# Performance work log

Hardware: AMD Instinct MI355X
Metric: run time of the kernel (lower is better)

The kernel has to match this reference:

```python
import jax, jax.numpy as jnp
import numpy as np

ALPHA_MEM = 0.95      # util.decayconst(tau_mem)
ALPHA_MEM_OUT = 0.95  # util.decayconst(tau_mem_out)
ALPHA_P = 0.99        # util.decayconst(tau_p)
SURR_SCALE = 100.0

@jax.custom_vjp
def spike(x):
    # Heaviside forward, surrogate gradient backward (SurrGradSpike)
    return (x > 0).astype(x.dtype)

def _spike_fwd(x):
    return spike(x), x

def _spike_bwd(x, g):
    return (g / (SURR_SCALE * jnp.abs(x) + 1.0) ** 2,)

spike.defvjp(_spike_fwd, _spike_bwd)


def setup_inputs() -> dict:
    B, T, N, NIN, NOUT, D = 64, 400, 1024, 128, 32, 3
    key = jax.random.key(0)
    ks = jax.random.split(key, 8)
    inputs = jax.random.normal(ks[0], (B, T, NIN), dtype=jnp.float32)
    w = jax.random.normal(ks[1], (N, N), dtype=jnp.float32) / np.sqrt(N).astype(np.float32)
    w_in = jax.random.normal(ks[2], (NIN, N), dtype=jnp.float32) * np.float32(0.3 / np.sqrt(NIN))
    w_out = jax.random.normal(ks[3], (N, NOUT), dtype=jnp.float32) * np.float32(0.3 / np.sqrt(N))
    w_signs = jnp.where(jax.random.uniform(ks[4], (N,)) < 0.8, 1.0, -1.0).astype(jnp.float32)
    dmap = (jax.random.uniform(ks[5], (D, N, N)) < 0.2).astype(jnp.float32)  # delay-wise connectivity mask
    p = jax.random.uniform(ks[6], (N,), minval=-0.5, maxval=0.5).astype(jnp.float32)
    delays = jnp.array([1, 2, 4], dtype=jnp.int32)
    return dict(inputs=inputs, w=w, w_in=w_in, w_out=w_out, w_signs=w_signs,
                dmap=dmap, p=p, delays=delays)


def _forward(inputs, w, w_in, w_out, w_signs, dmap, p, delays):
    B, T, _ = inputs.shape
    N = w.shape[0]
    L = int(np.max(np.asarray(delays))) + 1  # ring-buffer length (static)
    dtype = inputs.dtype

    inp = jnp.einsum('btc,cn->btn', inputs, w_in)           # epoch.input, (B,T,N)
    W = dmap * (w_signs[:, None] * jnp.abs(w))[None]        # (D,N,N)
    depr = (p < 0).astype(dtype)                            # p_depr_mask

    def step(carry, inp_t):
        mem, w_p, buf_out, buf_wp, t = carry
        out = spike(mem - 1.0)                              # mark_spikes
        buf_out = buf_out.at[t % L].set(out)                # record_state
        buf_wp = buf_wp.at[t % L].set(w_p)
        idx = (t - delays) % L
        syn_p = buf_out[idx] * (1.0 + buf_wp[idx])          # (D,B,N)
        syn = jnp.einsum('dbe,deo->bo', syn_p, W)
        w_p_new = w_p * ALPHA_P + out * p * (1.0 + depr * w_p)
        mem_new = ALPHA_MEM * mem + inp_t + syn - jax.lax.stop_gradient(out)
        return (mem_new, w_p_new, buf_out, buf_wp, t + 1), out

    z = jnp.zeros((B, N), dtype)
    bufs = jnp.zeros((L, B, N), dtype)
    carry0 = (z, z, bufs, bufs, jnp.int32(0))
    _, out_rec = jax.lax.scan(step, carry0, jnp.swapaxes(inp, 0, 1))  # (T,B,N)

    # compute_readout: leaky integrator over projected spikes
    h2 = jnp.einsum('tbn,no->tbo', out_rec, w_out)
    def ro_step(r, h):
        r = ALPHA_MEM_OUT * r + h
        return r, r
    _, readout = jax.lax.scan(ro_step, jnp.zeros((B, w_out.shape[1]), dtype), h2)
    return jnp.swapaxes(readout, 0, 1)                      # (B,T,NOUT)


def reference(inputs, w, w_in, w_out, w_signs, dmap, p, delays):
    return _forward(inputs, w, w_in, w_out, w_signs, dmap, p, delays)
```

## Files before the change

### kernel.cpp

```cpp
#include <hip/hip_runtime.h>
#include <cstdint>
#include <cstddef>

#define BB    64
#define TT    400
#define NN    1024
#define NIN   128
#define NOUT  32
#define DD    3
#define LL6   6
#define GG    16
#define BPG   4
#define NT    32
#define KK    3072
#define CAP   800

#define ALPHA_MEM     0.95f
#define ALPHA_MEM_OUT 0.95f
#define ALPHA_P       0.99f

__global__ void build_W(const float* __restrict__ w,
                        const float* __restrict__ w_signs,
                        const float* __restrict__ dmap,
                        float* __restrict__ W) {
    int idx = blockIdx.x * blockDim.x + threadIdx.x;
    if (idx >= DD * NN * NN) return;
    int en = idx % (NN * NN);
    int e  = en / NN;
    W[idx] = dmap[idx] * (w_signs[e] * fabsf(w[en]));
}

__global__ void build_csr(const float* __restrict__ W,
                          uint2* __restrict__ pack,
                          int*   __restrict__ ccnt) {
    const int col = blockIdx.x;
    const int tid = threadIdx.x;
    __shared__ int pref[256];
    __shared__ int total_s;

    int cnt = 0;
    #pragma unroll
    for (int i = 0; i < 12; ++i) {
        const float v = W[(size_t)(tid * 12 + i) * NN + col];
        cnt += (v != 0.0f) ? 1 : 0;
    }
    pref[tid] = cnt;
    __syncthreads();
    if (tid == 0) {
        int run = 0;
        for (int j = 0; j < 256; ++j) { int c = pref[j]; pref[j] = run; run += c; }
        total_s = run;
        ccnt[col] = (run > CAP) ? CAP : run;
    }
    __syncthreads();

    int ofs = pref[tid];
    #pragma unroll
    for (int i = 0; i < 12; ++i) {
        const int k = tid * 12 + i;
        const float v = W[(size_t)k * NN + col];
        if (v != 0.0f && ofs < CAP) {
            pack[(size_t)col * CAP + ofs] = make_uint2((unsigned)k, __float_as_uint(v));
            ++ofs;
        }
    }
    for (int s = total_s + tid; s < CAP; s += 256)
        pack[(size_t)col * CAP + s] = make_uint2(0u, 0u);
}

__global__ void gemm_in(const float* __restrict__ inputs,
                        const float* __restrict__ w_in,
                        float* __restrict__ inp) {
    int idx = blockIdx.x * blockDim.x + threadIdx.x;
    if (idx >= TT * BB * NN) return;
    int n  = idx & (NN - 1);
    int tb = idx >> 10;
    int b  = tb & 63;
    int t  = tb >> 6;
    const float* row = inputs + ((size_t)b * TT + t) * NIN;
    float acc = 0.0f;
    #pragma unroll 8
    for (int c = 0; c < NIN; ++c)
        acc = fmaf(row[c], w_in[c * NN + n], acc);
    inp[idx] = acc;
}

__global__ void zero_sc1(float* __restrict__ p, int n) {
    int i = blockIdx.x * blockDim.x + threadIdx.x;
    if (i < n)
        __hip_atomic_store(p + i, 0.0f, __ATOMIC_RELAXED, __HIP_MEMORY_SCOPE_AGENT);
}

__global__ __launch_bounds__(256, 2) void snn_scan(
    const float* __restrict__ inputs,
    const float* __restrict__ w_in,
    const float* __restrict__ w_out,
    const float* __restrict__ p,
    const int*   __restrict__ delays,
    const float* __restrict__ W,
    const float* __restrict__ w_raw,
    const float* __restrict__ w_signs,
    const float* __restrict__ dmap,
    float*       __restrict__ ring,
    int*         __restrict__ cnt,
    float*       __restrict__ hpart,
    const float* __restrict__ inp_pre,
    const uint2* __restrict__ pack,
    const int*   __restrict__ ccnt,
    float*       __restrict__ out,
    int use_pre, int use_W, int use_csr)
{
    __shared__ __align__(16) float sa[KK * BPG];
    __shared__ float w_out_s[32 * NOUT];
    __shared__ float spk_s[BPG * 32];
    __shared__ float s_sign[NN];
    __shared__ float s_in[BPG * NIN];

    const int bid  = blockIdx.x;
    const int g    = bid >> 5;
    const int tile = bid & 31;
    const int tid  = threadIdx.x;
    const int lane = tid & 63;
    const int wv   = tid >> 6;

    const bool st = (tid < BPG * 32);
    const int  sb = tid >> 5;
    const int  nl = tid & 31;

    const int gks = tid >> 3;
    const int gcg = tid & 7;

    const int colg = tid >> 3;
    const int sub  = tid & 7;

    float mem = 0.0f, wp = 0.0f, r = 0.0f;
    float pn = 0.0f, depr = 0.0f;
    if (st) { pn = p[tile * 32 + nl]; depr = (pn < 0.0f) ? 1.0f : 0.0f; }

    const int d0 = delays[0], d1 = delays[1], d2 = delays[2];

    for (int k = tid; k < 32 * NOUT; k += 256)
        w_out_s[k] = w_out[(tile * 32 + (k >> 5)) * NOUT + (k & 31)];
    if (!use_W)
        for (int k = tid; k < NN; k += 256) s_sign[k] = w_signs[k];
    __syncthreads();

    const float* Wt = W     + tile * 32 + gcg * 4;
    const float* Dt = dmap  + tile * 32 + gcg * 4;
    const float* Rt = w_raw + tile * 32 + gcg * 4;
    const uint2* Pk = pack  + (size_t)(tile * 32 + colg) * CAP;
    int niter = 0;
    if (use_csr) niter = (ccnt[tile * 32 + colg] + 7) >> 3;

    for (int t = 0; t < TT; ++t) {
        const int slot_w = t % LL6;
        const int s0 = (t - d0 + 2 * LL6) % LL6;
        const int s1 = (t - d1 + 2 * LL6) % LL6;
        const int s2 = (t - d2 + 2 * LL6) % LL6;

        bool  spk = false;
        float ia  = 0.0f;
        if (st) {
            spk = (mem - 1.0f) > 0.0f;
            const float a = spk ? (1.0f + wp) : 0.0f;
            __hip_atomic_store(ring + (((size_t)slot_w * BB + g * BPG + sb) << 10)
                                    + tile * 32 + nl,
                               a, __ATOMIC_RELAXED, __HIP_MEMORY_SCOPE_AGENT);
            wp = ALPHA_P * wp + (spk ? pn * (1.0f + depr * wp) : 0.0f);
            spk_s[tid] = spk ? 1.0f : 0.0f;
            if (use_pre)
                ia = inp_pre[((size_t)t * BB + g * BPG + sb) * NN + tile * 32 + nl];
        }
        if (!use_pre) {
            for (int k = tid; k < BPG * NIN; k += 256) {
                int b2 = k >> 7, c = k & 127;
                s_in[k] = inputs[((size_t)(g * BPG + b2) * TT + t) * NIN + c];
            }
        }
        __syncthreads();

        if (st) {
            float h = 0.0f;
            #pragma unroll
            for (int n2 = 0; n2 < 32; ++n2)
                h = fmaf(spk_s[sb * 32 + n2], w_out_s[n2 * 32 + nl], h);
            __hip_atomic_store(hpart + ((((size_t)(t & 1) * NT + tile) * BB)
                                        + g * BPG + sb) * NOUT + nl,
                               h, __ATOMIC_RELAXED, __HIP_MEMORY_SCOPE_AGENT);
            if (!use_pre) {
                #pragma unroll 8
                for (int c = 0; c < NIN; ++c)
                    ia = fmaf(s_in[sb * NIN + c], w_in[c * NN + tile * 32 + nl], ia);
            }
        }
        __syncthreads();

        if (tid == 0)
            __hip_atomic_fetch_add(&cnt[g * 32], 1, __ATOMIC_RELEASE,
                                   __HIP_MEMORY_SCOPE_AGENT);

        {
            const int b2 = lane >> 4;
            const int eo = lane & 15;
            #pragma unroll 16
            for (int i = 0; i < 48; ++i) {
                const int c  = i * 4 + wv;
                const int kl = c * 16 + eo;
                const int d  = kl >> 10;
                const int e  = kl & 1023;
                const int sl = (d == 0) ? s0 : ((d == 1) ? s1 : s2);
                const float v = __hip_atomic_load(
                    ring + (((size_t)sl * BB + g * BPG + b2) << 10) + e,
                    __ATOMIC_RELAXED, __HIP_MEMORY_SCOPE_AGENT);
                sa[kl * 4 + b2] = v;
            }
        }
        __syncthreads();

        if (tid == 0) {
            const int target = 32 * (t + 1);
            while (__hip_atomic_load(&cnt[g * 32], __ATOMIC_ACQUIRE,
                                     __HIP_MEMORY_SCOPE_AGENT) < target)
                __builtin_amdgcn_s_sleep(2);
        }
        __syncthreads();

        if (tile == 0 && st) {
            float h = 0.0f;
            #pragma unroll
            for (int k3 = 0; k3 < NT; ++k3)
                h += __hip_atomic_load(hpart + ((((size_t)(t & 1) * NT + k3) * BB)
                                                + g * BPG + sb) * NOUT + nl,
                                       __ATOMIC_RELAXED, __HIP_MEMORY_SCOPE_AGENT);
            r = ALPHA_MEM_OUT * r + h;
            out[((size_t)(g * BPG + sb) * TT + t) * NOUT + nl] = r;
        }

        if (use_csr) {
            float a0 = 0.0f, a1 = 0.0f, a2 = 0.0f, a3 = 0.0f;
            #pragma unroll 4
            for (int i = 0; i < niter; ++i) {
                const uint2 pv = Pk[i * 8 + sub];
                const float v  = __uint_as_float(pv.y);
                const float4 av = *(const float4*)&sa[pv.x << 2];
                a0 = fmaf(av.x, v, a0);
                a1 = fmaf(av.y, v, a1);
                a2 = fmaf(av.z, v, a2);
                a3 = fmaf(av.w, v, a3);
            }
            __syncthreads();

            float* red = sa;
            red[(colg * 4 + 0) * 9 + sub] = a0;
            red[(colg * 4 + 1) * 9 + sub] = a1;
            red[(colg * 4 + 2) * 9 + sub] = a2;
            red[(colg * 4 + 3) * 9 + sub] = a3;
            __syncthreads();

            if (st) {
                float syn = 0.0f;
                #pragma unroll
                for (int k2 = 0; k2 < 8; ++k2)
                    syn += red[(nl * 4 + sb) * 9 + k2];
                mem = ALPHA_MEM * mem + ia + syn - (spk ? 1.0f : 0.0f);
            }
            __syncthreads();
        } else {
            float4 acc0 = {0,0,0,0}, acc1 = {0,0,0,0}, acc2 = {0,0,0,0}, acc3 = {0,0,0,0};
            if (use_W) {
                #pragma unroll 8
                for (int i = 0; i < 96; ++i) {
                    const int kk = gks + (i << 5);
                    const float4 av = *(const float4*)&sa[kk << 2];
                    const float4 wv4 = *(const float4*)(Wt + ((size_t)kk << 10));
                    acc0.x = fmaf(av.x, wv4.x, acc0.x); acc0.y = fmaf(av.x, wv4.y, acc0.y);
                    acc0.z = fmaf(av.x, wv4.z, acc0.z); acc0.w = fmaf(av.x, wv4.w, acc0.w);
                    acc1.x = fmaf(av.y, wv4.x, acc1.x); acc1.y = fmaf(av.y, wv4.y, acc1.y);
                    acc1.z = fmaf(av.y, wv4.z, acc1.z); acc1.w = fmaf(av.y, wv4.w, acc1.w);
                    acc2.x = fmaf(av.z, wv4.x, acc2.x); acc2.y = fmaf(av.z, wv4.y, acc2.y);
                    acc2.z = fmaf(av.z, wv4.z, acc2.z); acc2.w = fmaf(av.z, wv4.w, acc2.w);
                    acc3.x = fmaf(av.w, wv4.x, acc3.x); acc3.y = fmaf(av.w, wv4.y, acc3.y);
                    acc3.z = fmaf(av.w, wv4.z, acc3.z); acc3.w = fmaf(av.w, wv4.w, acc3.w);
                }
            } else {
                #pragma unroll 2
                for (int i = 0; i < 96; ++i) {
                    const int kk = gks + (i << 5);
                    const int e  = kk & 1023;
                    const float sg = s_sign[e];
                    const float4 dm = *(const float4*)(Dt + ((size_t)kk << 10));
                    const float4 wr = *(const float4*)(Rt + ((size_t)e << 10));
                    float4 wv4;
                    wv4.x = dm.x * (sg * fabsf(wr.x));
                    wv4.y = dm.y * (sg * fabsf(wr.y));
                    wv4.z = dm.z * (sg * fabsf(wr.z));
                    wv4.w = dm.w * (sg * fabsf(wr.w));
                    const float4 av = *(const float4*)&sa[kk << 2];
                    acc0.x = fmaf(av.x, wv4.x, acc0.x); acc0.y = fmaf(av.x, wv4.y, acc0.y);
                    acc0.z = fmaf(av.x, wv4.z, acc0.z); acc0.w = fmaf(av.x, wv4.w, acc0.w);
                    acc1.x = fmaf(av.y, wv4.x, acc1.x); acc1.y = fmaf(av.y, wv4.y, acc1.y);
                    acc1.z = fmaf(av.y, wv4.z, acc1.z); acc1.w = fmaf(av.y, wv4.w, acc1.w);
                    acc2.x = fmaf(av.z, wv4.x, acc2.x); acc2.y = fmaf(av.z, wv4.y, acc2.y);
                    acc2.z = fmaf(av.z, wv4.z, acc2.z); acc2.w = fmaf(av.z, wv4.w, acc2.w);
                    acc3.x = fmaf(av.w, wv4.x, acc3.x); acc3.y = fmaf(av.w, wv4.y, acc3.y);
                    acc3.z = fmaf(av.w, wv4.z, acc3.z); acc3.w = fmaf(av.w, wv4.w, acc3.w);
                }
            }
            __syncthreads();

            float* red = sa;
            {
                const int o0 = gcg * 4;
                red[(0 * 32 + o0 + 0) * 33 + gks] = acc0.x;
                red[(0 * 32 + o0 + 1) * 33 + gks] = acc0.y;
                red[(0 * 32 + o0 + 2) * 33 + gks] = acc0.z;
                red[(0 * 32 + o0 + 3) * 33 + gks] = acc0.w;
                red[(1 * 32 + o0 + 0) * 33 + gks] = acc1.x;
                red[(1 * 32 + o0 + 1) * 33 + gks] = acc1.y;
                red[(1 * 32 + o0 + 2) * 33 + gks] = acc1.z;
                red[(1 * 32 + o0 + 3) * 33 + gks] = acc1.w;
                red[(2 * 32 + o0 + 0) * 33 + gks] = acc2.x;
                red[(2 * 32 + o0 + 1) * 33 + gks] = acc2.y;
                red[(2 * 32 + o0 + 2) * 33 + gks] = acc2.z;
                red[(2 * 32 + o0 + 3) * 33 + gks] = acc2.w;
                red[(3 * 32 + o0 + 0) * 33 + gks] = acc3.x;
                red[(3 * 32 + o0 + 1) * 33 + gks] = acc3.y;
                red[(3 * 32 + o0 + 2) * 33 + gks] = acc3.z;
                red[(3 * 32 + o0 + 3) * 33 + gks] = acc3.w;
            }
            __syncthreads();

            if (st) {
                float syn = 0.0f;
                #pragma unroll
                for (int k2 = 0; k2 < 32; ++k2)
                    syn += red[tid * 33 + k2];
                mem = ALPHA_MEM * mem + ia + syn - (spk ? 1.0f : 0.0f);
            }
            __syncthreads();
        }
    }
}

extern "C" void kernel_launch(void* const* d_in, const int* in_sizes, int n_in,
                              void* d_out, int out_size, void* d_ws, size_t ws_size,
                              hipStream_t stream) {
    const float* inputs  = (const float*)d_in[0];
    const float* w       = (const float*)d_in[1];
    const float* w_in    = (const float*)d_in[2];
    const float* w_out   = (const float*)d_in[3];
    const float* w_signs = (const float*)d_in[4];
    const float* dmap    = (const float*)d_in[5];
    const float* p       = (const float*)d_in[6];
    const int*   delays  = (const int*)d_in[7];
    float*       outp    = (float*)d_out;

    const size_t ring_f = (size_t)LL6 * BB * NN;
    const size_t cnt_f  = GG * 32;
    const size_t hp_f   = (size_t)2 * NT * BB * NOUT;
    const size_t W_f    = (size_t)DD * NN * NN;
    const size_t pre_f  = (size_t)TT * BB * NN;
    const size_t csr_f  = (size_t)NN * CAP * 2;
    const size_t cc_f   = NN;

    float* ws = (float*)d_ws;
    float* ring  = ws;
    int*   cntp  = (int*)(ws + ring_f);
    float* hpart = ws + ring_f + cnt_f;
    size_t used  = ring_f + cnt_f + hp_f;

    int use_W = 0, use_pre = 0, use_csr = 0;
    float *W = nullptr, *inp_pre = nullptr;
    uint2 *pack = nullptr;
    int   *ccnt = nullptr;
    if (ws_size >= (used + W_f) * 4)   { use_W = 1;   W = ws + used;       used += W_f; }
    if (ws_size >= (used + pre_f) * 4) { use_pre = 1; inp_pre = ws + used; used += pre_f; }
    if (use_W && ws_size >= (used + csr_f + cc_f) * 4) {
        use_csr = 1;
        pack = (uint2*)(ws + used); used += csr_f;
        ccnt = (int*)(ws + used);   used += cc_f;
    }

    if (use_W) {
        const int total = DD * NN * NN;
        build_W<<<(total + 255) / 256, 256, 0, stream>>>(w, w_signs, dmap, W);
    }
    if (use_csr)
        build_csr<<<NN, 256, 0, stream>>>(W, pack, ccnt);
    if (use_pre) {
        const int total = TT * BB * NN;
        gemm_in<<<(total + 255) / 256, 256, 0, stream>>>(inputs, w_in, inp_pre);
    }
    {
        const int total = (int)(ring_f + cnt_f);
        zero_sc1<<<(total + 255) / 256, 256, 0, stream>>>(ring, total);
    }

    void* args[] = {
        (void*)&inputs, (void*)&w_in, (void*)&w_out, (void*)&p, (void*)&delays,
        (void*)&W, (void*)&w, (void*)&w_signs, (void*)&dmap,
        (void*)&ring, (void*)&cntp, (void*)&hpart, (void*)&inp_pre, (void*)&pack,
        (void*)&ccnt, (void*)&outp, (void*)&use_pre, (void*)&use_W, (void*)&use_csr
    };
    hipError_t cerr = hipLaunchCooperativeKernel((const void*)snn_scan,
                               dim3(GG * NT), dim3(256), args, 0, stream);
    if (cerr != hipSuccess) {
        hipLaunchKernelGGL(snn_scan, dim3(GG * NT), dim3(256), 0, stream,
                           inputs, w_in, w_out, p, delays, W, w, w_signs, dmap,
                           ring, cntp, hpart, inp_pre, pack, ccnt, outp,
                           use_pre, use_W, use_csr);
    }
}
```

Measured before the change: 10.18 ms.

## Split batch across twice as many groups with two batches per block

```diff
diff --git a/kernel.cpp b/kernel.cpp
--- a/kernel.cpp
+++ b/kernel.cpp
@@ -9,8 +9,8 @@
 #define NOUT  32
 #define DD    3
 #define LL6   6
-#define GG    16
-#define BPG   4
+#define GG    32
+#define BPG   2
 #define NT    32
 #define KK    3072
 #define CAP   800
@@ -91,7 +91,7 @@
         __hip_atomic_store(p + i, 0.0f, __ATOMIC_RELAXED, __HIP_MEMORY_SCOPE_AGENT);
 }
 
-__global__ __launch_bounds__(256, 2) void snn_scan(
+__global__ __launch_bounds__(256, 4) void snn_scan(
     const float* __restrict__ inputs,
     const float* __restrict__ w_in,
     const float* __restrict__ w_out,
@@ -200,19 +200,19 @@
                                    __HIP_MEMORY_SCOPE_AGENT);
 
         {
-            const int b2 = lane >> 4;
-            const int eo = lane & 15;
-            #pragma unroll 16
-            for (int i = 0; i < 48; ++i) {
+            const int b2 = lane >> 5;
+            const int eo = lane & 31;
+            #pragma unroll 12
+            for (int i = 0; i < 24; ++i) {
                 const int c  = i * 4 + wv;
-                const int kl = c * 16 + eo;
+                const int kl = c * 32 + eo;
                 const int d  = kl >> 10;
                 const int e  = kl & 1023;
                 const int sl = (d == 0) ? s0 : ((d == 1) ? s1 : s2);
                 const float v = __hip_atomic_load(
                     ring + (((size_t)sl * BB + g * BPG + b2) << 10) + e,
                     __ATOMIC_RELAXED, __HIP_MEMORY_SCOPE_AGENT);
-                sa[kl * 4 + b2] = v;
+                sa[kl * 2 + b2] = v;
             }
         }
         __syncthreads();
@@ -237,50 +237,42 @@
         }
 
         if (use_csr) {
-            float a0 = 0.0f, a1 = 0.0f, a2 = 0.0f, a3 = 0.0f;
+            float a0 = 0.0f, a1 = 0.0f;
             #pragma unroll 4
             for (int i = 0; i < niter; ++i) {
                 const uint2 pv = Pk[i * 8 + sub];
                 const float v  = __uint_as_float(pv.y);
-                const float4 av = *(const float4*)&sa[pv.x << 2];
+                const float2 av = *(const float2*)&sa[pv.x << 1];
                 a0 = fmaf(av.x, v, a0);
                 a1 = fmaf(av.y, v, a1);
-                a2 = fmaf(av.z, v, a2);
-                a3 = fmaf(av.w, v, a3);
             }
             __syncthreads();
 
             float* red = sa;
-            red[(colg * 4 + 0) * 9 + sub] = a0;
-            red[(colg * 4 + 1) * 9 + sub] = a1;
-            red[(colg * 4 + 2) * 9 + sub] = a2;
-            red[(colg * 4 + 3) * 9 + sub] = a3;
+            red[(colg * 2 + 0) * 9 + sub] = a0;
+            red[(colg * 2 + 1) * 9 + sub] = a1;
             __syncthreads();
 
             if (st) {
                 float syn = 0.0f;
                 #pragma unroll
                 for (int k2 = 0; k2 < 8; ++k2)
-                    syn += red[(nl * 4 + sb) * 9 + k2];
+                    syn += red[(nl * 2 + sb) * 9 + k2];
                 mem = ALPHA_MEM * mem + ia + syn - (spk ? 1.0f : 0.0f);
             }
             __syncthreads();
         } else {
-            float4 acc0 = {0,0,0,0}, acc1 = {0,0,0,0}, acc2 = {0,0,0,0}, acc3 = {0,0,0,0};
+            float4 acc0 = {0,0,0,0}, acc1 = {0,0,0,0};
             if (use_W) {
                 #pragma unroll 8
                 for (int i = 0; i < 96; ++i) {
                     const int kk = gks + (i << 5);
-                    const float4 av = *(const float4*)&sa[kk << 2];
+                    const float2 av = *(const float2*)&sa[kk << 1];
                     const float4 wv4 = *(const float4*)(Wt + ((size_t)kk << 10));
                     acc0.x = fmaf(av.x, wv4.x, acc0.x); acc0.y = fmaf(av.x, wv4.y, acc0.y);
                     acc0.z = fmaf(av.x, wv4.z, acc0.z); acc0.w = fmaf(av.x, wv4.w, acc0.w);
                     acc1.x = fmaf(av.y, wv4.x, acc1.x); acc1.y = fmaf(av.y, wv4.y, acc1.y);
                     acc1.z = fmaf(av.y, wv4.z, acc1.z); acc1.w = fmaf(av.y, wv4.w, acc1.w);
-                    acc2.x = fmaf(av.z, wv4.x, acc2.x); acc2.y = fmaf(av.z, wv4.y, acc2.y);
-                    acc2.z = fmaf(av.z, wv4.z, acc2.z); acc2.w = fmaf(av.z, wv4.w, acc2.w);
-                    acc3.x = fmaf(av.w, wv4.x, acc3.x); acc3.y = fmaf(av.w, wv4.y, acc3.y);
-                    acc3.z = fmaf(av.w, wv4.z, acc3.z); acc3.w = fmaf(av.w, wv4.w, acc3.w);
                 }
             } else {
                 #pragma unroll 2
@@ -295,15 +287,11 @@
                     wv4.y = dm.y * (sg * fabsf(wr.y));
                     wv4.z = dm.z * (sg * fabsf(wr.z));
                     wv4.w = dm.w * (sg * fabsf(wr.w));
-                    const float4 av = *(const float4*)&sa[kk << 2];
+                    const float2 av = *(const float2*)&sa[kk << 1];
                     acc0.x = fmaf(av.x, wv4.x, acc0.x); acc0.y = fmaf(av.x, wv4.y, acc0.y);
                     acc0.z = fmaf(av.x, wv4.z, acc0.z); acc0.w = fmaf(av.x, wv4.w, acc0.w);
                     acc1.x = fmaf(av.y, wv4.x, acc1.x); acc1.y = fmaf(av.y, wv4.y, acc1.y);
                     acc1.z = fmaf(av.y, wv4.z, acc1.z); acc1.w = fmaf(av.y, wv4.w, acc1.w);
-                    acc2.x = fmaf(av.z, wv4.x, acc2.x); acc2.y = fmaf(av.z, wv4.y, acc2.y);
-                    acc2.z = fmaf(av.z, wv4.z, acc2.z); acc2.w = fmaf(av.z, wv4.w, acc2.w);
-                    acc3.x = fmaf(av.w, wv4.x, acc3.x); acc3.y = fmaf(av.w, wv4.y, acc3.y);
-                    acc3.z = fmaf(av.w, wv4.z, acc3.z); acc3.w = fmaf(av.w, wv4.w, acc3.w);
                 }
             }
             __syncthreads();
@@ -319,14 +307,6 @@
                 red[(1 * 32 + o0 + 1) * 33 + gks] = acc1.y;
                 red[(1 * 32 + o0 + 2) * 33 + gks] = acc1.z;
                 red[(1 * 32 + o0 + 3) * 33 + gks] = acc1.w;
-                red[(2 * 32 + o0 + 0) * 33 + gks] = acc2.x;
-                red[(2 * 32 + o0 + 1) * 33 + gks] = acc2.y;
-                red[(2 * 32 + o0 + 2) * 33 + gks] = acc2.z;
-                red[(2 * 32 + o0 + 3) * 33 + gks] = acc2.w;
-                red[(3 * 32 + o0 + 0) * 33 + gks] = acc3.x;
-                red[(3 * 32 + o0 + 1) * 33 + gks] = acc3.y;
-                red[(3 * 32 + o0 + 2) * 33 + gks] = acc3.z;
-                red[(3 * 32 + o0 + 3) * 33 + gks] = acc3.w;
             }
             __syncthreads();
 
@@ -334,7 +314,7 @@
                 float syn = 0.0f;
                 #pragma unroll
                 for (int k2 = 0; k2 < 32; ++k2)
-                    syn += red[tid * 33 + k2];
+                    syn += red[(sb * 32 + nl) * 33 + k2];
                 mem = ALPHA_MEM * mem + ia + syn - (spk ? 1.0f : 0.0f);
             }
             __syncthreads();
```

Result: slower. 15.88 ms (+55.9%).
